# Performance work log

Measured on AMD Instinct MI355X. Metric: run time of the kernel, lower is better.

The kernel has to match this reference:

```python
import jax, jax.numpy as jnp
import numpy as np


def setup_inputs() -> dict:
    key = jax.random.key(0)
    k1, k2, k3, k4, k5 = jax.random.split(key, 5)
    B, H, N, D = 32, 16, 1024, 128  # batch, heads, max_n_codes, head_dim
    transformer_t_1 = jax.random.normal(k1, (B, H, N, D), dtype=jnp.float32)
    transformer_t = jax.random.normal(k2, (B, H, N, D), dtype=jnp.float32)
    # valid-prefix padding vectors: first L entries nonzero, remainder zero
    lengths = jax.random.randint(k3, (B,), N // 2, N + 1)
    padding_t = (jnp.arange(N)[None, :] < lengths[:, None]).astype(jnp.int32)
    concat_w = jax.random.normal(k4, (1, 2 * D), dtype=jnp.float32) / np.sqrt(2 * D)
    concat_b = jax.random.normal(k5, (1,), dtype=jnp.float32) * 0.01
    return {
        "transformer_t_1": transformer_t_1,
        "transformer_t": transformer_t,
        "padding_t": padding_t,
        "max_n_codes": N,
        "concat_w": concat_w,
        "concat_b": concat_b,
    }


def reference(transformer_t_1, transformer_t, padding_t, max_n_codes, concat_w, concat_b):
    N = max_n_codes
    D = transformer_t.shape[-1]
    # create_padding_matrix: padd = index of first zero in padding row (else N);
    # mask positions n >= padd (True = masked out)
    iszero = padding_t == 0                      # [B, N]
    first0 = jnp.argmax(iszero, axis=1)          # [B]
    padd = jnp.where(iszero.any(axis=1), first0, N)
    mask = (jnp.arange(N)[None, :] >= padd[:, None])[:, None, :]  # [B, 1, N] -> bcast over heads

    # all_nodes_t_1: sum over node dim, broadcast back to every node
    s = transformer_t_1.sum(axis=2)              # [B, H, D]
    # concat Linear([all_nodes, transformer_t]) -> split weight into two halves
    w1 = concat_w[0, :D]
    w2 = concat_w[0, D:]
    score = (jnp.einsum('bhd,d->bh', s, w1)[:, :, None]
             + jnp.einsum('bhnd,d->bhn', transformer_t, w2)
             + concat_b[0])                      # [B, H, N]

    logits = jnp.where(mask, -jnp.inf, score)
    attn = jax.nn.softmax(logits, axis=-1)
    attn = jnp.where(mask, jnp.array(0.0, attn.dtype), attn)

    return transformer_t * attn[..., None] + transformer_t
```

## Files before the change

kernel.cpp:

```cpp
#include <hip/hip_runtime.h>

#define BB 32
#define HH 16
#define NN 1024
#define DD 128

__global__ __launch_bounds__(256) void score_kernel(const float* __restrict__ t,
                                                    const float* __restrict__ w2,
                                                    float* __restrict__ score) {
    const int tid  = threadIdx.x;
    const int wave = tid >> 6;
    const int lane = tid & 63;
    const int half = lane >> 5;
    const int l    = lane & 31;

    const float4 wv = ((const float4*)w2)[l];

    const long gbase = (long)blockIdx.x * 64 + (long)wave * 16 + half;
#pragma unroll
    for (int it = 0; it < 8; ++it) {
        const long g = gbase + (long)it * 2;
        const float4 tv = ((const float4*)(t + g * DD))[l];
        float p = tv.x * wv.x + tv.y * wv.y + tv.z * wv.z + tv.w * wv.w;
        p += __shfl_xor(p, 1);
        p += __shfl_xor(p, 2);
        p += __shfl_xor(p, 4);
        p += __shfl_xor(p, 8);
        p += __shfl_xor(p, 16);
        if (l == 0) score[g] = p;
    }
}

__global__ __launch_bounds__(256) void softmax_kernel(const int* __restrict__ padding,
                                                      float* __restrict__ score) {
    const int bh  = blockIdx.x;
    const int b   = bh >> 4;
    const int tid = threadIdx.x;

    __shared__ int   red_i[4];
    __shared__ float red_m[4];
    __shared__ float red_s[4];

    const int* pb = padding + b * NN;
    int lm = NN;
#pragma unroll
    for (int k = 0; k < 4; ++k) {
        const int i = tid + k * 256;
        if (pb[i] == 0) lm = min(lm, i);
    }
#pragma unroll
    for (int off = 32; off; off >>= 1) lm = min(lm, __shfl_xor(lm, off));
    if ((tid & 63) == 0) red_i[tid >> 6] = lm;
    __syncthreads();
    const int padd = min(min(red_i[0], red_i[1]), min(red_i[2], red_i[3]));

    float* row = score + (long)bh * NN;
    const float4 sc = ((const float4*)row)[tid];
    const int n0 = tid * 4;

    const float NEG = -3.4e38f;
    float m = (n0 + 0 < padd) ? sc.x : NEG;
    m = fmaxf(m, (n0 + 1 < padd) ? sc.y : NEG);
    m = fmaxf(m, (n0 + 2 < padd) ? sc.z : NEG);
    m = fmaxf(m, (n0 + 3 < padd) ? sc.w : NEG);
#pragma unroll
    for (int off = 32; off; off >>= 1) m = fmaxf(m, __shfl_xor(m, off));
    if ((tid & 63) == 0) red_m[tid >> 6] = m;
    __syncthreads();
    const float M = fmaxf(fmaxf(red_m[0], red_m[1]), fmaxf(red_m[2], red_m[3]));

    const float e0 = (n0 + 0 < padd) ? __expf(sc.x - M) : 0.f;
    const float e1 = (n0 + 1 < padd) ? __expf(sc.y - M) : 0.f;
    const float e2 = (n0 + 2 < padd) ? __expf(sc.z - M) : 0.f;
    const float e3 = (n0 + 3 < padd) ? __expf(sc.w - M) : 0.f;
    float s = e0 + e1 + e2 + e3;
#pragma unroll
    for (int off = 32; off; off >>= 1) s += __shfl_xor(s, off);
    if ((tid & 63) == 0) red_s[tid >> 6] = s;
    __syncthreads();
    const float S = red_s[0] + red_s[1] + red_s[2] + red_s[3];

    const float inv = (S > 0.f) ? (1.0f / S) : 0.f;
    float4 f4;
    f4.x = 1.f + e0 * inv;
    f4.y = 1.f + e1 * inv;
    f4.z = 1.f + e2 * inv;
    f4.w = 1.f + e3 * inv;
    ((float4*)row)[tid] = f4;
}

__global__ __launch_bounds__(256) void mul_kernel(const float* __restrict__ t,
                                                  const float* __restrict__ factor,
                                                  float* __restrict__ out) {
    const long g4 = (long)blockIdx.x * 256 + threadIdx.x;
    const float f = factor[g4 >> 5];
    float4 v = ((const float4*)t)[g4];
    v.x *= f; v.y *= f; v.z *= f; v.w *= f;
    ((float4*)out)[g4] = v;
}

extern "C" void kernel_launch(void* const* d_in, const int* in_sizes, int n_in,
                              void* d_out, int out_size, void* d_ws, size_t ws_size,
                              hipStream_t stream) {
    const float* t       = (const float*)d_in[1];
    const int*   padding = (const int*)d_in[2];
    const float* cw      = (const float*)d_in[4];
    float*       out     = (float*)d_out;
    float*       score   = (float*)d_ws;

    const int total_rows = BB * HH * NN;
    score_kernel<<<total_rows / 64, 256, 0, stream>>>(t, cw + DD, score);
    softmax_kernel<<<BB * HH, 256, 0, stream>>>(padding, score);
    const long total4 = (long)BB * HH * NN * DD / 4;
    mul_kernel<<<(int)(total4 / 256), 256, 0, stream>>>(t, score, out);
}
```

Measured before the change: 585.9 us.

## Fuse score, masked softmax and scaling into one per-row kernel

Replaces the three kernels (score, softmax, multiply) with a single kernel where each 1024-thread block handles one (batch, head) row. Scores are held in shared memory instead of a global workspace, and the second read of the row is intended to hit cache while it is still resident. Output writes use nontemporal stores. The trade-off is a grid of only 512 large blocks, which may limit latency hiding and parallelism.

```diff
diff --git a/kernel.cpp b/kernel.cpp
--- a/kernel.cpp
+++ b/kernel.cpp
@@ -5,98 +5,86 @@
 #define NN 1024
 #define DD 128
 
-__global__ __launch_bounds__(256) void score_kernel(const float* __restrict__ t,
-                                                    const float* __restrict__ w2,
-                                                    float* __restrict__ score) {
+typedef float fvec4 __attribute__((ext_vector_type(4)));
+
+__global__ __launch_bounds__(1024) void fused_kernel(const float* __restrict__ t,
+                                                     const int* __restrict__ padding,
+                                                     const float* __restrict__ w2,
+                                                     float* __restrict__ out) {
+    const int bh   = blockIdx.x;
+    const int b    = bh >> 4;
     const int tid  = threadIdx.x;
-    const int wave = tid >> 6;
+    const int wid  = tid >> 6;
     const int lane = tid & 63;
-    const int half = lane >> 5;
-    const int l    = lane & 31;
 
+    __shared__ float s_fac[NN];
+    __shared__ int   red_i[16];
+    __shared__ float red_f[16];
+
+    const float* trow = t + (long)bh * NN * DD;
+
+    int lm = (padding[b * NN + tid] == 0) ? tid : NN;
+#pragma unroll
+    for (int off = 32; off; off >>= 1) lm = min(lm, __shfl_xor(lm, off));
+    if (lane == 0) red_i[wid] = lm;
+
+    const int hw = tid >> 5;
+    const int l  = tid & 31;
     const float4 wv = ((const float4*)w2)[l];
-
-    const long gbase = (long)blockIdx.x * 64 + (long)wave * 16 + half;
-#pragma unroll
-    for (int it = 0; it < 8; ++it) {
-        const long g = gbase + (long)it * 2;
-        const float4 tv = ((const float4*)(t + g * DD))[l];
+#pragma unroll 4
+    for (int it = 0; it < 32; ++it) {
+        const int n = hw * 32 + it;
+        const float4 tv = ((const float4*)(trow + (long)n * DD))[l];
         float p = tv.x * wv.x + tv.y * wv.y + tv.z * wv.z + tv.w * wv.w;
         p += __shfl_xor(p, 1);
         p += __shfl_xor(p, 2);
         p += __shfl_xor(p, 4);
         p += __shfl_xor(p, 8);
         p += __shfl_xor(p, 16);
-        if (l == 0) score[g] = p;
+        if (l == 0) s_fac[n] = p;
     }
-}
+    __syncthreads();
 
-__global__ __launch_bounds__(256) void softmax_kernel(const int* __restrict__ padding,
-                                                      float* __restrict__ score) {
-    const int bh  = blockIdx.x;
-    const int b   = bh >> 4;
-    const int tid = threadIdx.x;
+    int padd = NN;
+#pragma unroll
+    for (int k = 0; k < 16; ++k) padd = min(padd, red_i[k]);
 
-    __shared__ int   red_i[4];
-    __shared__ float red_m[4];
-    __shared__ float red_s[4];
-
-    const int* pb = padding + b * NN;
-    int lm = NN;
-#pragma unroll
-    for (int k = 0; k < 4; ++k) {
-        const int i = tid + k * 256;
-        if (pb[i] == 0) lm = min(lm, i);
-    }
-#pragma unroll
-    for (int off = 32; off; off >>= 1) lm = min(lm, __shfl_xor(lm, off));
-    if ((tid & 63) == 0) red_i[tid >> 6] = lm;
-    __syncthreads();
-    const int padd = min(min(red_i[0], red_i[1]), min(red_i[2], red_i[3]));
-
-    float* row = score + (long)bh * NN;
-    const float4 sc = ((const float4*)row)[tid];
-    const int n0 = tid * 4;
-
+    const float sc  = s_fac[tid];
     const float NEG = -3.4e38f;
-    float m = (n0 + 0 < padd) ? sc.x : NEG;
-    m = fmaxf(m, (n0 + 1 < padd) ? sc.y : NEG);
-    m = fmaxf(m, (n0 + 2 < padd) ? sc.z : NEG);
-    m = fmaxf(m, (n0 + 3 < padd) ? sc.w : NEG);
+    float m = (tid < padd) ? sc : NEG;
 #pragma unroll
     for (int off = 32; off; off >>= 1) m = fmaxf(m, __shfl_xor(m, off));
-    if ((tid & 63) == 0) red_m[tid >> 6] = m;
+    if (lane == 0) red_f[wid] = m;
     __syncthreads();
-    const float M = fmaxf(fmaxf(red_m[0], red_m[1]), fmaxf(red_m[2], red_m[3]));
+    float M = NEG;
+#pragma unroll
+    for (int k = 0; k < 16; ++k) M = fmaxf(M, red_f[k]);
+    __syncthreads();
 
-    const float e0 = (n0 + 0 < padd) ? __expf(sc.x - M) : 0.f;
-    const float e1 = (n0 + 1 < padd) ? __expf(sc.y - M) : 0.f;
-    const float e2 = (n0 + 2 < padd) ? __expf(sc.z - M) : 0.f;
-    const float e3 = (n0 + 3 < padd) ? __expf(sc.w - M) : 0.f;
-    float s = e0 + e1 + e2 + e3;
+    const float e = (tid < padd) ? __expf(sc - M) : 0.f;
+    float s = e;
 #pragma unroll
     for (int off = 32; off; off >>= 1) s += __shfl_xor(s, off);
-    if ((tid & 63) == 0) red_s[tid >> 6] = s;
+    if (lane == 0) red_f[wid] = s;
     __syncthreads();
-    const float S = red_s[0] + red_s[1] + red_s[2] + red_s[3];
+    float S = 0.f;
+#pragma unroll
+    for (int k = 0; k < 16; ++k) S += red_f[k];
 
     const float inv = (S > 0.f) ? (1.0f / S) : 0.f;
-    float4 f4;
-    f4.x = 1.f + e0 * inv;
-    f4.y = 1.f + e1 * inv;
-    f4.z = 1.f + e2 * inv;
-    f4.w = 1.f + e3 * inv;
-    ((float4*)row)[tid] = f4;
-}
+    s_fac[tid] = 1.f + e * inv;
+    __syncthreads();
 
-__global__ __launch_bounds__(256) void mul_kernel(const float* __restrict__ t,
-                                                  const float* __restrict__ factor,
-                                                  float* __restrict__ out) {
-    const long g4 = (long)blockIdx.x * 256 + threadIdx.x;
-    const float f = factor[g4 >> 5];
-    float4 v = ((const float4*)t)[g4];
-    v.x *= f; v.y *= f; v.z *= f; v.w *= f;
-    ((float4*)out)[g4] = v;
+    const float4* t4 = (const float4*)trow;
+    fvec4*        o4 = (fvec4*)(out + (long)bh * NN * DD);
+#pragma unroll 4
+    for (int it = 0; it < 32; ++it) {
+        const int i4 = it * 1024 + tid;
+        const float f = s_fac[i4 >> 5];
+        float4 v = t4[i4];
+        fvec4 nv = {v.x * f, v.y * f, v.z * f, v.w * f};
+        __builtin_nontemporal_store(nv, o4 + i4);
+    }
 }
 
 extern "C" void kernel_launch(void* const* d_in, const int* in_sizes, int n_in,
@@ -106,11 +94,6 @@
     const int*   padding = (const int*)d_in[2];
     const float* cw      = (const float*)d_in[4];
     float*       out     = (float*)d_out;
-    float*       score   = (float*)d_ws;
 
-    const int total_rows = BB * HH * NN;
-    score_kernel<<<total_rows / 64, 256, 0, stream>>>(t, cw + DD, score);
-    softmax_kernel<<<BB * HH, 256, 0, stream>>>(padding, score);
-    const long total4 = (long)BB * HH * NN * DD / 4;
-    mul_kernel<<<(int)(total4 / 256), 256, 0, stream>>>(t, score, out);
+    fused_kernel<<<BB * HH, 1024, 0, stream>>>(t, padding, cw + DD, out);
 }
```

Result: no change. 576.8 us (-1.6%).
